# Optimization experiments

Hardware: AMD Instinct MI355X
Metric: run time of the kernel (lower is better)

## Reference

```python
import jax, jax.numpy as jnp
import numpy as np

DN = ('NCH', 'OIH', 'NCH')

def conv1d(x, w, b, pad):
    y = jax.lax.conv_general_dilated(x, w, (1,), [(pad, pad)], dimension_numbers=DN)
    return y if b is None else y + b[None, :, None]

def bn_eval(x, g, b, m, v, eps):
    s = g * jax.lax.rsqrt(v + eps)
    return x * s[None, :, None] + (b - m * s)[None, :, None]

def swish(x):
    return x * jax.nn.sigmoid(x)

def setup_inputs() -> dict:
    key = jax.random.key(0)
    ks = jax.random.split(key, 8)
    B, T, P = 16, 8192, 32
    inp = {
        'x': jax.random.normal(ks[0], (B, 1, T), jnp.float32),
        'conv_w': jax.random.normal(ks[1], (512, 1, 9), jnp.float32) * 0.1,
        'bn_g': jnp.ones((512,), jnp.float32),
        'bn_b': jnp.zeros((512,), jnp.float32),
        'bn_m': jnp.zeros((512,), jnp.float32),
        'bn_v': jnp.ones((512,), jnp.float32),
        'p1_w': jax.random.normal(ks[2], (P, 2, 31), jnp.float32) * 0.1,
        'p1_b': jnp.zeros((P,), jnp.float32),
        'pbn1_g': jnp.ones((P,), jnp.float32),
        'pbn1_b': jnp.zeros((P,), jnp.float32),
        'pbn1_m': jnp.zeros((P,), jnp.float32),
        'pbn1_v': jnp.ones((P,), jnp.float32),
        'p2_w': jax.random.normal(ks[3], (P, P, 15), jnp.float32) * 0.05,
        'p2_b': jnp.zeros((P,), jnp.float32),
        'pbn2_g': jnp.ones((P,), jnp.float32),
        'pbn2_b': jnp.zeros((P,), jnp.float32),
        'pbn2_m': jnp.zeros((P,), jnp.float32),
        'pbn2_v': jnp.ones((P,), jnp.float32),
        'p3_w': jax.random.normal(ks[4], (2, P, 15), jnp.float32) * 0.001,  # source scales last conv weight by 0.01
        'p3_b': jnp.full((2,), -np.log(2.0), jnp.float32),                 # source sets bias to -log(2)
        'norm_mean': jnp.ones((1,), jnp.float32),                           # eval-mode renorm buffer
    }
    return inp

def reference(x, conv_w, bn_g, bn_b, bn_m, bn_v,
              p1_w, p1_b, pbn1_g, pbn1_b, pbn1_m, pbn1_v,
              p2_w, p2_b, pbn2_g, pbn2_b, pbn2_m, pbn2_v,
              p3_w, p3_b, norm_mean):
    B, _, T = x.shape
    # main conv -> BN(eps=1e-3) -> GLU(dim=1); dropout is identity in eval
    h = conv1d(x, conv_w, None, 9 // 2)                 # [B, 512, T]
    h = bn_eval(h, bn_g, bn_b, bn_m, bn_v, 1e-3)
    a, g = jnp.split(h, 2, axis=1)
    features = a * jax.nn.sigmoid(g)                    # [B, 256, T]
    # predictor on cat([x, x*x])
    j = conv1d(jnp.concatenate([x, x * x], axis=1), p1_w, p1_b, 15)
    j = swish(bn_eval(j, pbn1_g, pbn1_b, pbn1_m, pbn1_v, 1e-5))
    j = conv1d(j, p2_w, p2_b, 7)
    j = swish(bn_eval(j, pbn2_g, pbn2_b, pbn2_m, pbn2_v, 1e-5))
    j = conv1d(j, p3_w, p3_b, 7)                        # [B, 2, T]
    weights = jax.nn.sigmoid(j[:, 0, :])                # [B, T]
    moves = jax.nn.sigmoid(j[:, 1, :])
    bmoves = moves
    moves = moves * norm_mean[0]                        # eval: renorm = norm_mean buffer
    # CIF-style dynamic pooling (row_pool), vectorized over batch
    feats = jnp.transpose(features, (0, 2, 1))          # [B, T, C]
    fw = feats * weights[..., None]
    poses = jnp.cumsum(jax.lax.stop_gradient(moves), axis=1)  # moves.detach() in source
    floors = jnp.floor(poses)
    w1 = 1.0 - (poses - floors)
    w2 = poses - floors
    fl = floors.astype(jnp.int32)
    ce = fl + 1
    Lmax = T + 2  # static bound: poses <= T so ceil index <= T+1
    C = fw.shape[2]
    def pool(fw_i, fl_i, ce_i, w1_i, w2_i):
        out = jnp.zeros((Lmax, C), fw_i.dtype)
        out = out.at[fl_i].add(w1_i[:, None] * fw_i)
        out = out.at[ce_i].add(w2_i[:, None] * fw_i)
        return out
    x_evs = jax.vmap(pool)(fw, fl, ce, w1, w2)          # [B, Lmax, C]
    lens = fl[:, -1] + 2                                 # int(ceils[-1]) + 1
    x_evs = jnp.transpose(x_evs, (0, 2, 1))             # [B, C, Lmax]
    pad = 3 - (Lmax % 3)
    x_evs = jnp.pad(x_evs, ((0, 0), (0, 0), (0, pad)))
    return x_evs, lens, bmoves, weights
```

## Files before the change

kernel.cpp:

```cpp
#include <hip/hip_runtime.h>
#include <math.h>

static constexpr int TT = 8192;
static constexpr int LFULL = 8196;
static constexpr int BSTRIDE = LFULL + 2;

static constexpr size_t XE_OFF   = 0;
static constexpr size_t LENS_OFF = (size_t)16*256*LFULL;
static constexpr size_t BM_OFF   = LENS_OFF + 16;
static constexpr size_t WT_OFF   = BM_OFF + (size_t)16*TT;

static constexpr size_t U_OFF     = 0;
static constexpr size_t V_OFF     = U_OFF + (size_t)16*32*TT;
static constexpr size_t MOVES_OFF = V_OFF + (size_t)16*32*TT;
static constexpr size_t C1_OFF    = MOVES_OFF + (size_t)16*TT;
static constexpr size_t C2_OFF    = C1_OFF + (size_t)16*TT;
static constexpr size_t BND_OFF   = U_OFF;

__device__ __forceinline__ float sig_(float z) { return 1.0f / (1.0f + __expf(-z)); }

__global__ __launch_bounds__(256) void k_conv1(
    const float* __restrict__ x,
    const float* __restrict__ p1w, const float* __restrict__ p1b,
    const float* __restrict__ g1, const float* __restrict__ b1,
    const float* __restrict__ m1, const float* __restrict__ v1,
    float* __restrict__ u)
{
    __shared__ float xin[2 * 320];
    __shared__ float w1t[2 * 992];
    const int tid = threadIdx.x;
    const int b = blockIdx.y;
    const int t0 = blockIdx.x * 256;

    for (int idx = tid; idx < 640; idx += 256) {
        int ci = idx / 320, xl = idx - ci * 320;
        int id = t0 - 15 + xl;
        float val = 0.f;
        if (xl < 286 && id >= 0 && id < TT) val = x[b * TT + id];
        xin[idx] = ci ? val * val : val;
    }
    for (int idx = tid; idx < 1984; idx += 256) {
        int c = idx / 62; int r = idx - c * 62; int ci = r / 31; int k = r - ci * 31;
        w1t[ci * 992 + c * 31 + k] = p1w[idx];
    }
    __syncthreads();

    const int tg = tid >> 5, c = tid & 31;
    float acc[32];
    const float bias = p1b[c];
#pragma unroll
    for (int i = 0; i < 32; ++i) acc[i] = bias;

    for (int h = 0; h < 4; ++h) {
        for (int ci = 0; ci < 2; ++ci) {
            float win[40];
            const float4* wp = (const float4*)(&xin[ci * 320 + tg * 32 + h * 8]);
#pragma unroll
            for (int r = 0; r < 10; ++r) {
                float4 q = wp[r];
                win[4*r] = q.x; win[4*r+1] = q.y; win[4*r+2] = q.z; win[4*r+3] = q.w;
            }
#pragma unroll
            for (int k = 0; k < 31; ++k) {
                float w = w1t[ci * 992 + c * 31 + k];
#pragma unroll
                for (int i = 0; i < 8; ++i) acc[h*8+i] = fmaf(w, win[i + k], acc[h*8+i]);
            }
        }
    }
    const float s = g1[c] * rsqrtf(v1[c] + 1e-5f);
    const float sh = b1[c] - m1[c] * s;
    float* up = &u[((size_t)(b * 32 + c)) * TT + t0 + tg * 32];
#pragma unroll
    for (int i = 0; i < 8; ++i) {
        float z0 = fmaf(acc[4*i+0], s, sh);
        float z1 = fmaf(acc[4*i+1], s, sh);
        float z2 = fmaf(acc[4*i+2], s, sh);
        float z3 = fmaf(acc[4*i+3], s, sh);
        ((float4*)up)[i] = make_float4(z0 * sig_(z0), z1 * sig_(z1), z2 * sig_(z2), z3 * sig_(z3));
    }
}

__global__ __launch_bounds__(256) void k_conv2(
    const float* __restrict__ u,
    const float* __restrict__ p2w, const float* __restrict__ p2b,
    const float* __restrict__ g2, const float* __restrict__ b2,
    const float* __restrict__ m2, const float* __restrict__ v2,
    float* __restrict__ vout)
{
    __shared__ float uld[16 * 272];
    __shared__ float w2t[16 * 256];
    const int tid = threadIdx.x;
    const int b = blockIdx.y;
    const int t0 = blockIdx.x * 256;
    const int ch = blockIdx.z;

    const int tg = tid >> 4, cl = tid & 15;
    const int c = ch * 16 + cl;
    float acc[16];
    const float bias = p2b[c];
#pragma unroll
    for (int i = 0; i < 16; ++i) acc[i] = bias;

    for (int h = 0; h < 2; ++h) {
        __syncthreads();
        for (int idx = tid; idx < 16 * 272; idx += 256) {
            int ci = idx / 272, tl = idx - ci * 272;
            int tgl = t0 - 7 + tl;
            float val = 0.f;
            if (tl < 270 && tgl >= 0 && tgl < TT) val = u[((size_t)(b * 32 + h * 16 + ci)) * TT + tgl];
            uld[idx] = val;
        }
        for (int idx = tid; idx < 16 * 256; idx += 256) {
            int ci = idx >> 8; int r = idx & 255; int cl2 = r >> 4; int k = r & 15;
            w2t[idx] = (k < 15) ? p2w[(ch * 16 + cl2) * 480 + (h * 16 + ci) * 15 + k] : 0.f;
        }
        __syncthreads();

        for (int ci = 0; ci < 16; ++ci) {
            float win[32];
            const float4* wp = (const float4*)(&uld[ci * 272 + tg * 16]);
#pragma unroll
            for (int r = 0; r < 8; ++r) {
                float4 q = wp[r];
                win[4*r] = q.x; win[4*r+1] = q.y; win[4*r+2] = q.z; win[4*r+3] = q.w;
            }
            float w[16];
            const float4* wqp = (const float4*)(&w2t[ci * 256 + cl * 16]);
#pragma unroll
            for (int r = 0; r < 4; ++r) {
                float4 q = wqp[r];
                w[4*r] = q.x; w[4*r+1] = q.y; w[4*r+2] = q.z; w[4*r+3] = q.w;
            }
#pragma unroll
            for (int k = 0; k < 15; ++k) {
#pragma unroll
                for (int i = 0; i < 16; ++i) acc[i] = fmaf(w[k], win[i + k], acc[i]);
            }
        }
    }
    const float s = g2[c] * rsqrtf(v2[c] + 1e-5f);
    const float sh = b2[c] - m2[c] * s;
    float o[16];
#pragma unroll
    for (int i = 0; i < 16; ++i) { float z = fmaf(acc[i], s, sh); o[i] = z * sig_(z); }
    float* vp = &vout[((size_t)(b * 32 + c)) * TT + t0 + tg * 16];
#pragma unroll
    for (int r = 0; r < 4; ++r)
        ((float4*)vp)[r] = make_float4(o[4*r], o[4*r+1], o[4*r+2], o[4*r+3]);
}

__global__ __launch_bounds__(256) void k_conv3(
    const float* __restrict__ vin,
    const float* __restrict__ p3w, const float* __restrict__ p3b,
    const float* __restrict__ nm,
    float* __restrict__ outw, float* __restrict__ outbm, float* __restrict__ moves)
{
    __shared__ float vld[32 * 276];
    __shared__ float wsh[960];
    const int tid = threadIdx.x;
    const int b = blockIdx.y;
    const int t0 = blockIdx.x * 256;

    for (int idx = tid; idx < 32 * 272; idx += 256) {
        int ci = idx / 272, tl = idx - ci * 272;
        int tg = t0 - 7 + tl;
        float val = 0.f;
        if (tl < 270 && tg >= 0 && tg < TT) val = vin[((size_t)(b * 32 + ci)) * TT + tg];
        vld[ci * 276 + tl] = val;
    }
    for (int idx = tid; idx < 960; idx += 256) wsh[idx] = p3w[idx];
    __syncthreads();

    const int g = tid >> 2;
    const int q = tid & 3;
    float acc[8];
#pragma unroll
    for (int i = 0; i < 8; ++i) acc[i] = 0.f;

#pragma unroll
    for (int i = 0; i < 8; ++i) {
        const int ci = q + 4 * i;
        float win[20];
        const float4* wp = (const float4*)(&vld[ci * 276 + g * 4]);
#pragma unroll
        for (int r = 0; r < 5; ++r) {
            float4 v4 = wp[r];
            win[4*r] = v4.x; win[4*r+1] = v4.y; win[4*r+2] = v4.z; win[4*r+3] = v4.w;
        }
        const float* w0 = &wsh[ci * 15];
        const float* w1 = &wsh[480 + ci * 15];
#pragma unroll
        for (int k = 0; k < 15; ++k) {
            const float a = w0[k], gw = w1[k];
#pragma unroll
            for (int tt = 0; tt < 4; ++tt) {
                acc[tt]     = fmaf(a,  win[k + tt], acc[tt]);
                acc[4 + tt] = fmaf(gw, win[k + tt], acc[4 + tt]);
            }
        }
    }
#pragma unroll
    for (int i = 0; i < 8; ++i) {
        acc[i] += __shfl_xor(acc[i], 1, 64);
        acc[i] += __shfl_xor(acc[i], 2, 64);
    }
    if (q == 0) {
        const float nmv = nm[0];
        const float b0 = p3b[0], b1 = p3b[1];
        const int t = t0 + g * 4;
        float4 wv = make_float4(sig_(acc[0]+b0), sig_(acc[1]+b0), sig_(acc[2]+b0), sig_(acc[3]+b0));
        float4 bm = make_float4(sig_(acc[4]+b1), sig_(acc[5]+b1), sig_(acc[6]+b1), sig_(acc[7]+b1));
        float4 mv = make_float4(bm.x*nmv, bm.y*nmv, bm.z*nmv, bm.w*nmv);
        *(float4*)&outw[b * TT + t]  = wv;
        *(float4*)&outbm[b * TT + t] = bm;
        *(float4*)&moves[b * TT + t] = mv;
    }
}

__global__ __launch_bounds__(1024) void k_scan(
    const float* __restrict__ moves, const float* __restrict__ wts,
    float* __restrict__ coef1, float* __restrict__ coef2,
    int* __restrict__ bnd, float* __restrict__ lens)
{
    __shared__ float wsum[16];
    const int tid = threadIdx.x;
    const int b = blockIdx.x;
    const int lane = tid & 63, wv = tid >> 6;
    float carry = 0.f;

    int* bb = &bnd[b * BSTRIDE];
    for (int i = tid; i < BSTRIDE; i += 1024) bb[i] = TT;
    if (tid == 0) { bb[0] = 0; bb[1] = 0; }
    __syncthreads();

    const float4* mv4 = (const float4*)&moves[b * TT];
    const float4* wt4 = (const float4*)&wts[b * TT];
    float4* c14 = (float4*)&coef1[b * TT];
    float4* c24 = (float4*)&coef2[b * TT];

    for (int chunk = 0; chunk < 2; ++chunk) {
        const int idx = chunk * 1024 + tid;
        float4 m = mv4[idx];
        const float s = m.x + m.y + m.z + m.w;
        float v = s;
#pragma unroll
        for (int off = 1; off < 64; off <<= 1) {
            float n = __shfl_up(v, off, 64);
            if (lane >= off) v += n;
        }
        if (lane == 63) wsum[wv] = v;
        __syncthreads();
        float pre = carry;
        for (int w = 0; w < wv; ++w) pre += wsum[w];
        float tot = 0.f;
#pragma unroll
        for (int w = 0; w < 16; ++w) tot += wsum[w];
        const float base = pre + (v - s);
        const float p0 = base + m.x;
        const float p1 = p0 + m.y;
        const float p2 = p1 + m.z;
        const float p3 = p2 + m.w;
        const float4 w4 = wt4[idx];
        const float fr0 = p0 - floorf(p0), fr1 = p1 - floorf(p1);
        const float fr2 = p2 - floorf(p2), fr3 = p3 - floorf(p3);
        c14[idx] = make_float4((1.f - fr0) * w4.x, (1.f - fr1) * w4.y,
                               (1.f - fr2) * w4.z, (1.f - fr3) * w4.w);
        c24[idx] = make_float4(fr0 * w4.x, fr1 * w4.y, fr2 * w4.z, fr3 * w4.w);
        {
            int lf = (int)floorf(base) + 1;
            const int lfe = (int)floorf(p3);
            const int tbase = idx << 2;
            for (; lf <= lfe; ++lf) {
                const float lff = (float)lf;
                int t = tbase;
                if (p0 >= lff) { }
                else if (p1 >= lff) t += 1;
                else if (p2 >= lff) t += 2;
                else t += 3;
                if (lf + 1 < BSTRIDE) bb[lf + 1] = t;
            }
        }
        if (chunk == 1 && tid == 1023) lens[b] = floorf(p3) + 2.0f;
        carry += tot;
        __syncthreads();
    }
}

static constexpr int LTILE = 32;
static constexpr int CHK = 256;
static constexpr int NPOOLX = (LFULL + LTILE - 1) / LTILE;

__global__ __launch_bounds__(256) void k_pool(
    const float* __restrict__ x,
    const float* __restrict__ cw,
    const float* __restrict__ bng, const float* __restrict__ bnb,
    const float* __restrict__ bnm, const float* __restrict__ bnv,
    const float* __restrict__ coef1, const float* __restrict__ coef2,
    const int* __restrict__ bnd, const float* __restrict__ lens,
    float* __restrict__ xevs)
{
    __shared__ float out_lds[256 * 33];
    __shared__ float4 xl4[68];
    __shared__ float4 c1l4[CHK / 4], c2l4[CHK / 4];
    __shared__ int lbs[LTILE + 2];
    float* xl = (float*)xl4;
    float* c1l = (float*)c1l4;
    float* c2l = (float*)c2l4;

    const int tid = threadIdx.x;
    const int b = blockIdx.y;

    if (blockIdx.x >= NPOOLX) {
        const int zx = blockIdx.x - NPOOLX;
        const int zs = (((int)lens[b]) + 15) & ~15;
        if (zs >= LFULL) return;
        const int n4 = (LFULL - zs) >> 2;
        const float4 z = make_float4(0.f, 0.f, 0.f, 0.f);
        for (int r = 0; r < 4; ++r) {
            float4* row4 = (float4*)&xevs[((size_t)(b * 256 + zx * 4 + r)) * LFULL + zs];
            for (int i = tid; i < n4; i += 256) row4[i] = z;
        }
        return;
    }

    const int l0 = blockIdx.x * LTILE;
    const int LTa = min(LTILE, LFULL - l0);

    if (tid < LTa + 2) lbs[tid] = bnd[b * BSTRIDE + l0 + tid];
    __syncthreads();

    const int t_lo = lbs[0];
    const int t_hi = lbs[LTa + 1];
    if (t_lo >= t_hi) return;

    const size_t rowbase = (size_t)b * 256 * LFULL + l0;

#pragma unroll
    for (int li = 0; li < 33; ++li) out_lds[tid * 33 + li] = 0.f;

    const int c = tid;
    float wa[9], wg[9];
#pragma unroll
    for (int k = 0; k < 9; ++k) { wa[k] = cw[c * 9 + k]; wg[k] = cw[(c + 256) * 9 + k]; }
    const float sa = bng[c] * rsqrtf(bnv[c] + 1e-3f);
    const float sha = bnb[c] - bnm[c] * sa;
    const float sg = bng[c + 256] * rsqrtf(bnv[c + 256] + 1e-3f);
    const float shg = bnb[c + 256] - bnm[c + 256] * sg;

    const float* xg = &x[b * TT];
    const float* c1g = &coef1[b * TT];
    const float* c2g = &coef2[b * TT];

    float accA = 0.f, accB = 0.f;
    int j = 0;
    int nb = lbs[1];

    for (int cs = t_lo; cs < t_hi; cs += CHK) {
        const int ce = min(cs + CHK, t_hi);
        const int len = ce - cs;
        __syncthreads();
        for (int idx = tid; idx < len + 12; idx += 256) {
            int id = cs - 4 + idx;
            xl[idx] = (id >= 0 && id < TT) ? xg[id] : 0.f;
        }
        if (tid < len) { c1l[tid] = c1g[cs + tid]; c2l[tid] = c2g[cs + tid]; }
        __syncthreads();

        const int len4 = len >> 2;
        for (int g = 0; g < len4; ++g) {
            float4 A = xl4[g], Bq = xl4[g + 1], Cq = xl4[g + 2];
            float w[12] = {A.x, A.y, A.z, A.w, Bq.x, Bq.y, Bq.z, Bq.w, Cq.x, Cq.y, Cq.z, Cq.w};
            float f[4];
#pragma unroll
            for (int i = 0; i < 4; ++i) {
                float s0 = 0.f, s1 = 0.f;
#pragma unroll
                for (int k = 0; k < 9; ++k) { s0 = fmaf(wa[k], w[i + k], s0); s1 = fmaf(wg[k], w[i + k], s1); }
                const float av = fmaf(s0, sa, sha);
                const float gv = fmaf(s1, sg, shg);
                f[i] = av * sig_(gv);
            }
            float4 c1v = c1l4[g], c2v = c2l4[g];
            const float c1a[4] = {c1v.x, c1v.y, c1v.z, c1v.w};
            const float c2a[4] = {c2v.x, c2v.y, c2v.z, c2v.w};
            const int tb = cs + (g << 2);
#pragma unroll
            for (int i = 0; i < 4; ++i) {
                const int t = tb + i;
                while (t >= nb) {
                    int li = j - 1;
                    if (li >= 0 && li < LTa) out_lds[c * 33 + li] = accA;
                    accA = accB; accB = 0.f;
                    ++j;
                    nb = lbs[j + 1];
                }
                accA = fmaf(c1a[i], f[i], accA);
                accB = fmaf(c2a[i], f[i], accB);
            }
        }
        for (int t = cs + (len4 << 2); t < ce; ++t) {
            const int il = t - cs;
            float s0 = 0.f, s1 = 0.f;
#pragma unroll
            for (int k = 0; k < 9; ++k) { float xv = xl[il + k]; s0 = fmaf(wa[k], xv, s0); s1 = fmaf(wg[k], xv, s1); }
            const float av = fmaf(s0, sa, sha);
            const float gv = fmaf(s1, sg, shg);
            const float f0 = av * sig_(gv);
            while (t >= nb) {
                int li = j - 1;
                if (li >= 0 && li < LTa) out_lds[c * 33 + li] = accA;
                accA = accB; accB = 0.f;
                ++j;
                nb = lbs[j + 1];
            }
            accA = fmaf(c1l[il], f0, accA);
            accB = fmaf(c2l[il], f0, accB);
        }
    }
    {
        int li = j - 1;
        if (li >= 0 && li < LTa) out_lds[c * 33 + li] = accA;
    }
    __syncthreads();

#pragma unroll
    for (int it = 0; it < 8; ++it) {
        int idx4 = it * 256 + tid;
        int cc = idx4 >> 3, q = (idx4 & 7) << 2;
        if (q < LTa) {
            float4 o;
            o.x = out_lds[cc * 33 + q + 0];
            o.y = out_lds[cc * 33 + q + 1];
            o.z = out_lds[cc * 33 + q + 2];
            o.w = out_lds[cc * 33 + q + 3];
            *(float4*)(&xevs[rowbase + (size_t)cc * LFULL + q]) = o;
        }
    }
}

extern "C" void kernel_launch(void* const* d_in, const int* in_sizes, int n_in,
                              void* d_out, int out_size, void* d_ws, size_t ws_size,
                              hipStream_t stream) {
    (void)in_sizes; (void)n_in; (void)out_size; (void)ws_size;
    const float* x      = (const float*)d_in[0];
    const float* conv_w = (const float*)d_in[1];
    const float* bn_g   = (const float*)d_in[2];
    const float* bn_b   = (const float*)d_in[3];
    const float* bn_m   = (const float*)d_in[4];
    const float* bn_v   = (const float*)d_in[5];
    const float* p1_w   = (const float*)d_in[6];
    const float* p1_b   = (const float*)d_in[7];
    const float* pbn1_g = (const float*)d_in[8];
    const float* pbn1_b = (const float*)d_in[9];
    const float* pbn1_m = (const float*)d_in[10];
    const float* pbn1_v = (const float*)d_in[11];
    const float* p2_w   = (const float*)d_in[12];
    const float* p2_b   = (const float*)d_in[13];
    const float* pbn2_g = (const float*)d_in[14];
    const float* pbn2_b = (const float*)d_in[15];
    const float* pbn2_m = (const float*)d_in[16];
    const float* pbn2_v = (const float*)d_in[17];
    const float* p3_w   = (const float*)d_in[18];
    const float* p3_b   = (const float*)d_in[19];
    const float* nm     = (const float*)d_in[20];

    float* out = (float*)d_out;
    float* ws  = (float*)d_ws;
    float* u     = ws + U_OFF;
    float* v     = ws + V_OFF;
    float* moves = ws + MOVES_OFF;
    float* coef1 = ws + C1_OFF;
    float* coef2 = ws + C2_OFF;
    int*   bnd   = (int*)(ws + BND_OFF);
    float* xevs  = out + XE_OFF;
    float* lens  = out + LENS_OFF;
    float* bmv   = out + BM_OFF;
    float* wts   = out + WT_OFF;

    k_conv1<<<dim3(32, 16), 256, 0, stream>>>(x, p1_w, p1_b, pbn1_g, pbn1_b, pbn1_m, pbn1_v, u);
    k_conv2<<<dim3(32, 16, 2), 256, 0, stream>>>(u, p2_w, p2_b, pbn2_g, pbn2_b, pbn2_m, pbn2_v, v);
    k_conv3<<<dim3(32, 16), 256, 0, stream>>>(v, p3_w, p3_b, nm, wts, bmv, moves);
    k_scan<<<16, 1024, 0, stream>>>(moves, wts, coef1, coef2, bnd, lens);
    k_pool<<<dim3(NPOOLX + 64, 16), 256, 0, stream>>>(
        x, conv_w, bn_g, bn_b, bn_m, bn_v, coef1, coef2, bnd, lens, xevs);
}
```

Measured before the change: 339.4 us.

## Fuse conv1 into conv2 with halo recompute and use nontemporal output stores

Merges the first and second predictor convolutions into one kernel. Each block recomputes the conv1+BN+swish activations for its time tile plus halo into shared memory, so the intermediate u tensor is never written to or read back from global memory. The cost is that conv1 is computed twice, once per channel-half block along z, and more shared memory is used per block, which may lower occupancy. The pool kernel's output and zero-fill stores also become nontemporal, so the large xevs write bypasses the caches.

```diff
diff --git a/kernel.cpp b/kernel.cpp
--- a/kernel.cpp
+++ b/kernel.cpp
@@ -19,132 +19,121 @@
 
 __device__ __forceinline__ float sig_(float z) { return 1.0f / (1.0f + __expf(-z)); }
 
-__global__ __launch_bounds__(256) void k_conv1(
+typedef float f4v __attribute__((ext_vector_type(4)));
+__device__ __forceinline__ void nt_store4(float* p, float a, float b, float c, float d) {
+    f4v v = {a, b, c, d};
+    __builtin_nontemporal_store(v, (f4v*)p);
+}
+
+__global__ __launch_bounds__(256) void k_conv12(
     const float* __restrict__ x,
     const float* __restrict__ p1w, const float* __restrict__ p1b,
     const float* __restrict__ g1, const float* __restrict__ b1,
     const float* __restrict__ m1, const float* __restrict__ v1,
-    float* __restrict__ u)
-{
-    __shared__ float xin[2 * 320];
-    __shared__ float w1t[2 * 992];
-    const int tid = threadIdx.x;
-    const int b = blockIdx.y;
-    const int t0 = blockIdx.x * 256;
-
-    for (int idx = tid; idx < 640; idx += 256) {
-        int ci = idx / 320, xl = idx - ci * 320;
-        int id = t0 - 15 + xl;
-        float val = 0.f;
-        if (xl < 286 && id >= 0 && id < TT) val = x[b * TT + id];
-        xin[idx] = ci ? val * val : val;
-    }
-    for (int idx = tid; idx < 1984; idx += 256) {
-        int c = idx / 62; int r = idx - c * 62; int ci = r / 31; int k = r - ci * 31;
-        w1t[ci * 992 + c * 31 + k] = p1w[idx];
-    }
-    __syncthreads();
-
-    const int tg = tid >> 5, c = tid & 31;
-    float acc[32];
-    const float bias = p1b[c];
-#pragma unroll
-    for (int i = 0; i < 32; ++i) acc[i] = bias;
-
-    for (int h = 0; h < 4; ++h) {
-        for (int ci = 0; ci < 2; ++ci) {
-            float win[40];
-            const float4* wp = (const float4*)(&xin[ci * 320 + tg * 32 + h * 8]);
-#pragma unroll
-            for (int r = 0; r < 10; ++r) {
-                float4 q = wp[r];
-                win[4*r] = q.x; win[4*r+1] = q.y; win[4*r+2] = q.z; win[4*r+3] = q.w;
-            }
-#pragma unroll
-            for (int k = 0; k < 31; ++k) {
-                float w = w1t[ci * 992 + c * 31 + k];
-#pragma unroll
-                for (int i = 0; i < 8; ++i) acc[h*8+i] = fmaf(w, win[i + k], acc[h*8+i]);
-            }
-        }
-    }
-    const float s = g1[c] * rsqrtf(v1[c] + 1e-5f);
-    const float sh = b1[c] - m1[c] * s;
-    float* up = &u[((size_t)(b * 32 + c)) * TT + t0 + tg * 32];
-#pragma unroll
-    for (int i = 0; i < 8; ++i) {
-        float z0 = fmaf(acc[4*i+0], s, sh);
-        float z1 = fmaf(acc[4*i+1], s, sh);
-        float z2 = fmaf(acc[4*i+2], s, sh);
-        float z3 = fmaf(acc[4*i+3], s, sh);
-        ((float4*)up)[i] = make_float4(z0 * sig_(z0), z1 * sig_(z1), z2 * sig_(z2), z3 * sig_(z3));
-    }
-}
-
-__global__ __launch_bounds__(256) void k_conv2(
-    const float* __restrict__ u,
     const float* __restrict__ p2w, const float* __restrict__ p2b,
     const float* __restrict__ g2, const float* __restrict__ b2,
     const float* __restrict__ m2, const float* __restrict__ v2,
     float* __restrict__ vout)
 {
-    __shared__ float uld[16 * 272];
-    __shared__ float w2t[16 * 256];
+    __shared__ float xin[320];
+    __shared__ float w1t[2 * 992];
+    __shared__ float uld[32 * 276];
+    __shared__ float w2t[32 * 256];
     const int tid = threadIdx.x;
     const int b = blockIdx.y;
     const int t0 = blockIdx.x * 256;
     const int ch = blockIdx.z;
 
+    for (int idx = tid; idx < 320; idx += 256) {
+        int id = t0 - 22 + idx;
+        xin[idx] = (id >= 0 && id < TT) ? x[b * TT + id] : 0.f;
+    }
+    for (int idx = tid; idx < 1984; idx += 256) {
+        int c = idx / 62; int r = idx - c * 62; int ci = r / 31; int k = r - ci * 31;
+        w1t[ci * 992 + c * 31 + k] = p1w[idx];
+    }
+    for (int idx = tid; idx < 32 * 256; idx += 256) {
+        int ci = idx >> 8; int r = idx & 255; int cl2 = r >> 4; int k = r & 15;
+        w2t[idx] = (k < 15) ? p2w[(ch * 16 + cl2) * 480 + ci * 15 + k] : 0.f;
+    }
+    __syncthreads();
+
+    {
+        const int cB = tid & 31, pg = tid >> 5;
+        const float s1v = g1[cB] * rsqrtf(v1[cB] + 1e-5f);
+        const float sh1 = b1[cB] - m1[cB] * s1v;
+        const float bias1 = p1b[cB];
+        const int base = pg * 36;
+        const float* wA = &w1t[cB * 31];
+        const float* wB = &w1t[992 + cB * 31];
+#pragma unroll
+        for (int h = 0; h < 5; ++h) {
+            const int off = h * 8;
+            const int len = (h < 4) ? 8 : 4;
+            const int nld = (h < 4) ? 10 : 9;
+            float win[40], wsq[40];
+            const float4* xp = (const float4*)(&xin[base + off]);
+            for (int r = 0; r < nld; ++r) {
+                float4 q = xp[r];
+                win[4*r] = q.x; win[4*r+1] = q.y; win[4*r+2] = q.z; win[4*r+3] = q.w;
+            }
+            for (int i = 0; i < 4 * nld; ++i) wsq[i] = win[i] * win[i];
+            float acc[8];
+#pragma unroll
+            for (int i = 0; i < 8; ++i) acc[i] = bias1;
+#pragma unroll
+            for (int k = 0; k < 31; ++k) {
+                const float a = wA[k], bw = wB[k];
+                for (int i = 0; i < len; ++i) {
+                    acc[i] = fmaf(a, win[i + k], acc[i]);
+                    acc[i] = fmaf(bw, wsq[i + k], acc[i]);
+                }
+            }
+            for (int i = 0; i < len; ++i) {
+                const int tl = base + off + i;
+                if (tl < 270) {
+                    const float z = fmaf(acc[i], s1v, sh1);
+                    uld[cB * 276 + tl] = z * sig_(z);
+                }
+            }
+        }
+    }
+    __syncthreads();
+
     const int tg = tid >> 4, cl = tid & 15;
-    const int c = ch * 16 + cl;
-    float acc[16];
-    const float bias = p2b[c];
-#pragma unroll
-    for (int i = 0; i < 16; ++i) acc[i] = bias;
-
-    for (int h = 0; h < 2; ++h) {
-        __syncthreads();
-        for (int idx = tid; idx < 16 * 272; idx += 256) {
-            int ci = idx / 272, tl = idx - ci * 272;
-            int tgl = t0 - 7 + tl;
-            float val = 0.f;
-            if (tl < 270 && tgl >= 0 && tgl < TT) val = u[((size_t)(b * 32 + h * 16 + ci)) * TT + tgl];
-            uld[idx] = val;
-        }
-        for (int idx = tid; idx < 16 * 256; idx += 256) {
-            int ci = idx >> 8; int r = idx & 255; int cl2 = r >> 4; int k = r & 15;
-            w2t[idx] = (k < 15) ? p2w[(ch * 16 + cl2) * 480 + (h * 16 + ci) * 15 + k] : 0.f;
-        }
-        __syncthreads();
-
-        for (int ci = 0; ci < 16; ++ci) {
-            float win[32];
-            const float4* wp = (const float4*)(&uld[ci * 272 + tg * 16]);
-#pragma unroll
-            for (int r = 0; r < 8; ++r) {
-                float4 q = wp[r];
-                win[4*r] = q.x; win[4*r+1] = q.y; win[4*r+2] = q.z; win[4*r+3] = q.w;
-            }
-            float w[16];
-            const float4* wqp = (const float4*)(&w2t[ci * 256 + cl * 16]);
-#pragma unroll
-            for (int r = 0; r < 4; ++r) {
-                float4 q = wqp[r];
-                w[4*r] = q.x; w[4*r+1] = q.y; w[4*r+2] = q.z; w[4*r+3] = q.w;
-            }
-#pragma unroll
-            for (int k = 0; k < 15; ++k) {
-#pragma unroll
-                for (int i = 0; i < 16; ++i) acc[i] = fmaf(w[k], win[i + k], acc[i]);
-            }
-        }
-    }
-    const float s = g2[c] * rsqrtf(v2[c] + 1e-5f);
-    const float sh = b2[c] - m2[c] * s;
+    const int c2 = ch * 16 + cl;
+    float acc2[16];
+    const float bias2 = p2b[c2];
+#pragma unroll
+    for (int i = 0; i < 16; ++i) acc2[i] = bias2;
+
+    for (int ci = 0; ci < 32; ++ci) {
+        float win[32];
+        const float4* wp = (const float4*)(&uld[ci * 276 + tg * 16]);
+#pragma unroll
+        for (int r = 0; r < 8; ++r) {
+            float4 q = wp[r];
+            win[4*r] = q.x; win[4*r+1] = q.y; win[4*r+2] = q.z; win[4*r+3] = q.w;
+        }
+        float w[16];
+        const float4* wqp = (const float4*)(&w2t[ci * 256 + cl * 16]);
+#pragma unroll
+        for (int r = 0; r < 4; ++r) {
+            float4 q = wqp[r];
+            w[4*r] = q.x; w[4*r+1] = q.y; w[4*r+2] = q.z; w[4*r+3] = q.w;
+        }
+#pragma unroll
+        for (int k = 0; k < 15; ++k) {
+#pragma unroll
+            for (int i = 0; i < 16; ++i) acc2[i] = fmaf(w[k], win[i + k], acc2[i]);
+        }
+    }
+    const float s = g2[c2] * rsqrtf(v2[c2] + 1e-5f);
+    const float sh = b2[c2] - m2[c2] * s;
     float o[16];
 #pragma unroll
-    for (int i = 0; i < 16; ++i) { float z = fmaf(acc[i], s, sh); o[i] = z * sig_(z); }
-    float* vp = &vout[((size_t)(b * 32 + c)) * TT + t0 + tg * 16];
+    for (int i = 0; i < 16; ++i) { float z = fmaf(acc2[i], s, sh); o[i] = z * sig_(z); }
+    float* vp = &vout[((size_t)(b * 32 + c2)) * TT + t0 + tg * 16];
 #pragma unroll
     for (int r = 0; r < 4; ++r)
         ((float4*)vp)[r] = make_float4(o[4*r], o[4*r+1], o[4*r+2], o[4*r+3]);
@@ -316,10 +305,9 @@
         const int zs = (((int)lens[b]) + 15) & ~15;
         if (zs >= LFULL) return;
         const int n4 = (LFULL - zs) >> 2;
-        const float4 z = make_float4(0.f, 0.f, 0.f, 0.f);
         for (int r = 0; r < 4; ++r) {
-            float4* row4 = (float4*)&xevs[((size_t)(b * 256 + zx * 4 + r)) * LFULL + zs];
-            for (int i = tid; i < n4; i += 256) row4[i] = z;
+            float* row = &xevs[((size_t)(b * 256 + zx * 4 + r)) * LFULL + zs];
+            for (int i = tid; i < n4; i += 256) nt_store4(row + 4 * i, 0.f, 0.f, 0.f, 0.f);
         }
         return;
     }
@@ -429,12 +417,9 @@
         int idx4 = it * 256 + tid;
         int cc = idx4 >> 3, q = (idx4 & 7) << 2;
         if (q < LTa) {
-            float4 o;
-            o.x = out_lds[cc * 33 + q + 0];
-            o.y = out_lds[cc * 33 + q + 1];
-            o.z = out_lds[cc * 33 + q + 2];
-            o.w = out_lds[cc * 33 + q + 3];
-            *(float4*)(&xevs[rowbase + (size_t)cc * LFULL + q]) = o;
+            nt_store4(&xevs[rowbase + (size_t)cc * LFULL + q],
+                      out_lds[cc * 33 + q + 0], out_lds[cc * 33 + q + 1],
+                      out_lds[cc * 33 + q + 2], out_lds[cc * 33 + q + 3]);
         }
     }
 }
@@ -467,7 +452,6 @@
 
     float* out = (float*)d_out;
     float* ws  = (float*)d_ws;
-    float* u     = ws + U_OFF;
     float* v     = ws + V_OFF;
     float* moves = ws + MOVES_OFF;
     float* coef1 = ws + C1_OFF;
@@ -478,8 +462,9 @@
     float* bmv   = out + BM_OFF;
     float* wts   = out + WT_OFF;
 
-    k_conv1<<<dim3(32, 16), 256, 0, stream>>>(x, p1_w, p1_b, pbn1_g, pbn1_b, pbn1_m, pbn1_v, u);
-    k_conv2<<<dim3(32, 16, 2), 256, 0, stream>>>(u, p2_w, p2_b, pbn2_g, pbn2_b, pbn2_m, pbn2_v, v);
+    k_conv12<<<dim3(32, 16, 2), 256, 0, stream>>>(
+        x, p1_w, p1_b, pbn1_g, pbn1_b, pbn1_m, pbn1_v,
+        p2_w, p2_b, pbn2_g, pbn2_b, pbn2_m, pbn2_v, v);
     k_conv3<<<dim3(32, 16), 256, 0, stream>>>(v, p3_w, p3_b, nm, wts, bmv, moves);
     k_scan<<<16, 1024, 0, stream>>>(moves, wts, coef1, coef2, bnd, lens);
     k_pool<<<dim3(NPOOLX + 64, 16), 256, 0, stream>>>(
```

New measurement: 337.0 us. No clear change (-0.7%).
